# Kernel optimization log

Hardware: AMD Instinct MI355X
Metric: run time of the kernel (lower is better)

The kernel has to match this reference:

```python
import jax, jax.numpy as jnp
import numpy as np

N_HEADS = 8  # must match init_kwargs n_heads


def _shift(x, dy, dx):
    """out[..., y, x] = x[..., y+dy, x+dx], zero-padded outside. Replaces im2col gather / col2im scatter."""
    H, W = x.shape[-2], x.shape[-1]
    py0, py1 = max(dy, 0), max(-dy, 0)
    px0, px1 = max(dx, 0), max(-dx, 0)
    xp = jnp.pad(x, [(0, 0)] * (x.ndim - 2) + [(py1, py0), (px1, px0)])
    return xp[..., py1 + dy:py1 + dy + H, px1 + dx:px1 + dx + W]


def setup_inputs() -> dict:
    key = jax.random.key(0)
    k1, k2, k3 = jax.random.split(key, 3)
    N, D, H, W = 8, 256, 128, 128
    V = jax.random.normal(k1, (N, D, H, W), dtype=jnp.float32)
    K = jax.random.normal(k2, (N, D, H, W), dtype=jnp.float32)
    Q = jax.random.normal(k3, (N, D, H, W), dtype=jnp.float32)
    mask = jnp.ones((N, 1, H, W), dtype=jnp.float32)
    return {"V": V, "K": K, "Q": Q, "ksize": 5, "dilation": 1, "mask": mask}


def reference(V, K, Q, ksize, dilation, mask):
    N, D, H, W = Q.shape
    Dv = V.shape[1]
    nh = N_HEADS
    h_dim = D // nh
    dv_h = Dv // nh
    pad = (ksize // 2) * dilation
    offsets = [(i * dilation - pad, j * dilation - pad)
               for i in range(ksize) for j in range(ksize)]  # P = ksize**2 window positions

    # per-head QK scores for each window offset: score_p = sum_c K[y+dy, x+dx] * Q[y, x]
    Qh = Q.reshape(N, nh, h_dim, H, W)
    scores = []
    for (dy, dx) in offsets:
        Ks = _shift(K, dy, dx).reshape(N, nh, h_dim, H, W)
        scores.append(jnp.sum(Ks * Qh, axis=2))  # (N, nh, H, W)
    scores = jnp.stack(scores, axis=0)  # (P, N, nh, H, W)

    # softmax over window positions (dim 2 in the torch code), then mask
    att = jax.nn.softmax(scores, axis=0)
    m = mask.reshape(N, 1, H, W)[:, 0]  # (N, H, W)
    att = att * m[None, :, None, :, :]

    # diffuse V: value at (y, x) weighted by att[p] scatters to (y+dy, x+dx) (col2im add)
    Vh = V.reshape(N, nh, dv_h, H, W)
    out = jnp.zeros((N, nh, dv_h, H, W), dtype=V.dtype)
    for p, (dy, dx) in enumerate(offsets):
        contrib = Vh * att[p][:, :, None]  # (N, nh, dv_h, H, W)
        out = out + _shift(contrib, -dy, -dx)
    return out.reshape(N, Dv, H, W)
```

## Files before the change

### kernel.cpp

```cpp
#include <hip/hip_runtime.h>
#include <hip/hip_bf16.h>

typedef __hip_bfloat16 bf16;

#define N_     8
#define NH     8
#define HD     32
#define HW     (128 * 128)
#define H_     128
#define W_     128
#define P_     25
#define TY     8
#define RG     12
#define PITCH  136
#define CH     4
#define NCH    (HD / CH)
#define NPLANE (N_ * NH * HW)

static __device__ __forceinline__ unsigned short f2bf(float f) {
  bf16 b = __float2bfloat16(f);
  return *(unsigned short*)&b;
}

__global__ __launch_bounds__(256) void attn_kernel(
    const float* __restrict__ Kp, const float* __restrict__ Qp,
    const float* __restrict__ maskp, bf16* __restrict__ att) {
  __shared__ float L[CH][RG][PITCH];

  const int tid = threadIdx.x;
  const int y0 = blockIdx.x * TY, nh = blockIdx.y;
  const int ty = tid >> 5, g = tid & 31;
  const int gy = y0 + ty, gx0 = 4 * g;
  const float* KU = Kp + (size_t)nh * (HD * HW);
  const float* QU = Qp + (size_t)nh * (HD * HW);

  const int scol = tid & 127;
  const int sr0  = tid >> 7;
  int gofs[6]; bool okr[6];
#pragma unroll
  for (int j = 0; j < 6; ++j) {
    const int ky = y0 - 2 + sr0 + 2 * j;
    okr[j] = (unsigned)ky < H_;
    gofs[j] = okr[j] ? ky * W_ + scol : 0;
  }

  if (tid < 192) {
    const int ch = tid / 48, rem = tid % 48, r = rem >> 2, c = rem & 3;
    L[ch][r][c < 2 ? c : c + 128] = 0.f;
  }

  float s[P_][4];
#pragma unroll
  for (int p = 0; p < P_; ++p)
#pragma unroll
    for (int px = 0; px < 4; ++px) s[p][px] = 0.f;

  float t[6][CH];
#pragma unroll
  for (int j = 0; j < 6; ++j)
#pragma unroll
    for (int ch = 0; ch < CH; ++ch)
      t[j][ch] = okr[j] ? KU[gofs[j] + ch * HW] : 0.f;

#pragma unroll 1
  for (int kc = 0; kc < NCH; ++kc) {
    const int c0 = kc * CH;
    float q[CH][4];
#pragma unroll
    for (int ch = 0; ch < CH; ++ch) {
      float4 qv = *(const float4*)(QU + (c0 + ch) * HW + gy * W_ + gx0);
      q[ch][0] = qv.x; q[ch][1] = qv.y; q[ch][2] = qv.z; q[ch][3] = qv.w;
    }

    if (kc) __syncthreads();
#pragma unroll
    for (int j = 0; j < 6; ++j)
#pragma unroll
      for (int ch = 0; ch < CH; ++ch)
        L[ch][sr0 + 2 * j][scol + 2] = t[j][ch];
    __syncthreads();

    if (kc < NCH - 1) {
      const int cn = (kc + 1) * CH;
#pragma unroll
      for (int j = 0; j < 6; ++j)
#pragma unroll
        for (int ch = 0; ch < CH; ++ch)
          t[j][ch] = okr[j] ? KU[gofs[j] + (cn + ch) * HW] : 0.f;
    }

#pragma unroll
    for (int ch = 0; ch < CH; ++ch)
#pragma unroll
      for (int dyi = 0; dyi < 5; ++dyi) {
        const float* rp = &L[ch][ty + dyi][4 * g];
        float4 ra = *(const float4*)rp;
        float4 rb = *(const float4*)(rp + 4);
        float r[8] = {ra.x, ra.y, ra.z, ra.w, rb.x, rb.y, rb.z, rb.w};
#pragma unroll
        for (int dxi = 0; dxi < 5; ++dxi)
#pragma unroll
          for (int px = 0; px < 4; ++px)
            s[dyi * 5 + dxi][px] += r[px + dxi] * q[ch][px];
      }
  }

  float4 mv = *(const float4*)(maskp + (size_t)(nh >> 3) * HW + gy * W_ + gx0);
  float mvv[4] = {mv.x, mv.y, mv.z, mv.w};
  float inv[4];
#pragma unroll
  for (int px = 0; px < 4; ++px) {
    float m = s[0][px];
#pragma unroll
    for (int p = 1; p < P_; ++p) m = fmaxf(m, s[p][px]);
    float sum = 0.f;
#pragma unroll
    for (int p = 0; p < P_; ++p) { float e = __expf(s[p][px] - m); s[p][px] = e; sum += e; }
    inv[px] = mvv[px] / sum;
  }
  unsigned short* A = (unsigned short*)att;
  const size_t pixbase = (size_t)nh * HW + gy * W_ + gx0;
#pragma unroll
  for (int p = 0; p < P_; ++p) {
    uint2 o;
    o.x = (unsigned)f2bf(s[p][0] * inv[0]) | ((unsigned)f2bf(s[p][1] * inv[1]) << 16);
    o.y = (unsigned)f2bf(s[p][2] * inv[2]) | ((unsigned)f2bf(s[p][3] * inv[3]) << 16);
    *(uint2*)(A + (size_t)p * NPLANE + pixbase) = o;
  }
}

__global__ __launch_bounds__(256) void diffuse_kernel(
    const float* __restrict__ Vp, const bf16* __restrict__ att,
    float* __restrict__ out) {
  __shared__ float L[CH][RG][PITCH];

  const int tid = threadIdx.x;
  const int y0 = blockIdx.x * TY, nh = blockIdx.y;
  const int ty = tid >> 5, g = tid & 31;
  const int gy = y0 + ty, gx0 = 4 * g;
  const float* VU = Vp + (size_t)nh * (HD * HW);
  float* OU = out + (size_t)nh * (HD * HW);

  const int scol = tid & 127;
  const int sr0  = tid >> 7;
  int gofs[6]; bool okr[6];
#pragma unroll
  for (int j = 0; j < 6; ++j) {
    const int ky = y0 - 2 + sr0 + 2 * j;
    okr[j] = (unsigned)ky < H_;
    gofs[j] = okr[j] ? ky * W_ + scol : 0;
  }

  float t[6][CH];
#pragma unroll
  for (int j = 0; j < 6; ++j)
#pragma unroll
    for (int ch = 0; ch < CH; ++ch)
      t[j][ch] = okr[j] ? VU[gofs[j] + ch * HW] : 0.f;

  const unsigned short* A = (const unsigned short*)att;
  unsigned mxl[5], mxh[5];
#pragma unroll
  for (int exi = 0; exi < 5; ++exi) {
    bool o0 = (unsigned)(gx0 + 0 + exi - 2) < W_;
    bool o1 = (unsigned)(gx0 + 1 + exi - 2) < W_;
    bool o2 = (unsigned)(gx0 + 2 + exi - 2) < W_;
    bool o3 = (unsigned)(gx0 + 3 + exi - 2) < W_;
    mxl[exi] = (o0 ? 0xFFFFu : 0u) | (o1 ? 0xFFFF0000u : 0u);
    mxh[exi] = (o2 ? 0xFFFFu : 0u) | (o3 ? 0xFFFF0000u : 0u);
  }
  uint2 wp[P_];
#pragma unroll
  for (int j = 0; j < P_; ++j) {
    const int eyi = j / 5, exi = j % 5;
    const int ys = gy + eyi - 2;
    uint2 v; v.x = 0u; v.y = 0u;
    if ((unsigned)ys < H_) {
      const size_t base = (size_t)(24 - j) * NPLANE + (size_t)nh * HW +
                          (size_t)(ys * W_) + (gx0 + exi - 2);
      if (exi == 2) {
        v = *(const uint2*)(A + base);
      } else if ((exi & 1) == 0) {
        v.x = *(const unsigned*)(A + base);
        v.y = *(const unsigned*)(A + base + 2);
      } else {
        unsigned u0 = *(const unsigned*)(A + base - 1);
        unsigned u1 = *(const unsigned*)(A + base + 1);
        unsigned u2 = *(const unsigned*)(A + base + 3);
        v.x = (u0 >> 16) | (u1 << 16);
        v.y = (u1 >> 16) | (u2 << 16);
      }
    }
    v.x &= mxl[exi]; v.y &= mxh[exi];
    wp[j] = v;
  }

  if (tid < 192) {
    const int ch = tid / 48, rem = tid % 48, r = rem >> 2, c = rem & 3;
    L[ch][r][c < 2 ? c : c + 128] = 0.f;
  }

#pragma unroll 1
  for (int kc = 0; kc < NCH; ++kc) {
    if (kc) __syncthreads();
#pragma unroll
    for (int j = 0; j < 6; ++j)
#pragma unroll
      for (int ch = 0; ch < CH; ++ch)
        L[ch][sr0 + 2 * j][scol + 2] = t[j][ch];
    __syncthreads();

    if (kc < NCH - 1) {
      const int cn = (kc + 1) * CH;
#pragma unroll
      for (int j = 0; j < 6; ++j)
#pragma unroll
        for (int ch = 0; ch < CH; ++ch)
          t[j][ch] = okr[j] ? VU[gofs[j] + (cn + ch) * HW] : 0.f;
    }

    float acc[CH][4];
#pragma unroll
    for (int ch = 0; ch < CH; ++ch)
#pragma unroll
      for (int px = 0; px < 4; ++px) acc[ch][px] = 0.f;

#pragma unroll
    for (int eyi = 0; eyi < 5; ++eyi) {
      float vr[CH][8];
#pragma unroll
      for (int ch = 0; ch < CH; ++ch) {
        const float* rp = &L[ch][ty + eyi][4 * g];
        float4 ra = *(const float4*)rp;
        float4 rb = *(const float4*)(rp + 4);
        vr[ch][0] = ra.x; vr[ch][1] = ra.y; vr[ch][2] = ra.z; vr[ch][3] = ra.w;
        vr[ch][4] = rb.x; vr[ch][5] = rb.y; vr[ch][6] = rb.z; vr[ch][7] = rb.w;
      }
#pragma unroll
      for (int exi = 0; exi < 5; ++exi) {
        const uint2 w2 = wp[eyi * 5 + exi];
        float wf[4];
        wf[0] = __uint_as_float(w2.x << 16);
        wf[1] = __uint_as_float(w2.x & 0xFFFF0000u);
        wf[2] = __uint_as_float(w2.y << 16);
        wf[3] = __uint_as_float(w2.y & 0xFFFF0000u);
#pragma unroll
        for (int ch = 0; ch < CH; ++ch)
#pragma unroll
          for (int px = 0; px < 4; ++px)
            acc[ch][px] += wf[px] * vr[ch][px + exi];
      }
    }

    const int c0 = kc * CH;
#pragma unroll
    for (int ch = 0; ch < CH; ++ch) {
      float4 o = make_float4(acc[ch][0], acc[ch][1], acc[ch][2], acc[ch][3]);
      *(float4*)(OU + (c0 + ch) * HW + gy * W_ + gx0) = o;
    }
  }
}

extern "C" void kernel_launch(void* const* d_in, const int* in_sizes, int n_in,
                              void* d_out, int out_size, void* d_ws, size_t ws_size,
                              hipStream_t stream) {
  const float* V    = (const float*)d_in[0];
  const float* K    = (const float*)d_in[1];
  const float* Q    = (const float*)d_in[2];
  const float* mask = (const float*)d_in[5];

  bf16* att = (bf16*)d_ws;

  dim3 grid(H_ / TY, N_ * NH);
  attn_kernel<<<grid, 256, 0, stream>>>(K, Q, mask, att);
  diffuse_kernel<<<grid, 256, 0, stream>>>(V, att, (float*)d_out);
}
```

Baseline: 165.7 us.

## Use packed fp16 dot2 for QK scores and drop register prefetch of K

The score kernel now converts K and Q channel pairs to packed fp16 and accumulates scores with v_dot2 instructions, halving the shared-memory tile and the FMA count for the QK dot product. It also removes the register double-buffered prefetch of the next K chunk, loading K synchronously each iteration, and hoists the mask load to the start. This reduces ALU and LDS work but lowers score precision (fp16 with round-toward-zero) and may expose global load latency that the prefetch used to hide.

```diff
diff --git a/kernel.cpp b/kernel.cpp
--- a/kernel.cpp
+++ b/kernel.cpp
@@ -2,6 +2,8 @@
 #include <hip/hip_bf16.h>
 
 typedef __hip_bfloat16 bf16;
+typedef __attribute__((ext_vector_type(2))) __fp16    fp16x2;
+typedef __attribute__((ext_vector_type(2))) _Float16  half2t;
 
 #define N_     8
 #define NH     8
@@ -21,11 +23,20 @@
   bf16 b = __float2bfloat16(f);
   return *(unsigned short*)&b;
 }
+union h2u {
+  unsigned u; fp16x2 f; half2t h;
+};
+static __device__ __forceinline__ unsigned pk2u(float a, float b) {
+  h2u x; x.f = __builtin_amdgcn_cvt_pkrtz(a, b); return x.u;
+}
+static __device__ __forceinline__ half2t u2h(unsigned v) {
+  h2u x; x.u = v; return x.h;
+}
 
 __global__ __launch_bounds__(256) void attn_kernel(
     const float* __restrict__ Kp, const float* __restrict__ Qp,
     const float* __restrict__ maskp, bf16* __restrict__ att) {
-  __shared__ float L[CH][RG][PITCH];
+  __shared__ unsigned Lh[2][RG][PITCH];
 
   const int tid = threadIdx.x;
   const int y0 = blockIdx.x * TY, nh = blockIdx.y;
@@ -44,9 +55,9 @@
     gofs[j] = okr[j] ? ky * W_ + scol : 0;
   }
 
-  if (tid < 192) {
-    const int ch = tid / 48, rem = tid % 48, r = rem >> 2, c = rem & 3;
-    L[ch][r][c < 2 ? c : c + 128] = 0.f;
+  if (tid < 96) {
+    const int cp = tid / 48, rem = tid % 48, r = rem >> 2, c = rem & 3;
+    Lh[cp][r][c < 2 ? c : c + 128] = 0u;
   }
 
   float s[P_][4];
@@ -55,57 +66,56 @@
 #pragma unroll
     for (int px = 0; px < 4; ++px) s[p][px] = 0.f;
 
-  float t[6][CH];
-#pragma unroll
-  for (int j = 0; j < 6; ++j)
-#pragma unroll
-    for (int ch = 0; ch < CH; ++ch)
-      t[j][ch] = okr[j] ? KU[gofs[j] + ch * HW] : 0.f;
+  float4 mv = *(const float4*)(maskp + (size_t)(nh >> 3) * HW + gy * W_ + gx0);
 
 #pragma unroll 1
   for (int kc = 0; kc < NCH; ++kc) {
-    const int c0 = kc * CH;
+    const int cb = kc * CH;
+    if (kc) __syncthreads();
+
+    float t[6][CH];
+#pragma unroll
+    for (int j = 0; j < 6; ++j)
+#pragma unroll
+      for (int c = 0; c < CH; ++c)
+        t[j][c] = okr[j] ? KU[gofs[j] + (cb + c) * HW] : 0.f;
+#pragma unroll
+    for (int j = 0; j < 6; ++j)
+#pragma unroll
+      for (int m = 0; m < 2; ++m)
+        Lh[m][sr0 + 2 * j][scol + 2] = pk2u(t[j][2 * m], t[j][2 * m + 1]);
+    __syncthreads();
+
     float q[CH][4];
 #pragma unroll
-    for (int ch = 0; ch < CH; ++ch) {
-      float4 qv = *(const float4*)(QU + (c0 + ch) * HW + gy * W_ + gx0);
-      q[ch][0] = qv.x; q[ch][1] = qv.y; q[ch][2] = qv.z; q[ch][3] = qv.w;
-    }
-
-    if (kc) __syncthreads();
-#pragma unroll
-    for (int j = 0; j < 6; ++j)
-#pragma unroll
-      for (int ch = 0; ch < CH; ++ch)
-        L[ch][sr0 + 2 * j][scol + 2] = t[j][ch];
-    __syncthreads();
-
-    if (kc < NCH - 1) {
-      const int cn = (kc + 1) * CH;
-#pragma unroll
-      for (int j = 0; j < 6; ++j)
-#pragma unroll
-        for (int ch = 0; ch < CH; ++ch)
-          t[j][ch] = okr[j] ? KU[gofs[j] + (cn + ch) * HW] : 0.f;
-    }
-
-#pragma unroll
-    for (int ch = 0; ch < CH; ++ch)
+    for (int c = 0; c < CH; ++c) {
+      float4 qv = *(const float4*)(QU + (cb + c) * HW + gy * W_ + gx0);
+      q[c][0] = qv.x; q[c][1] = qv.y; q[c][2] = qv.z; q[c][3] = qv.w;
+    }
+    unsigned qp[2][4];
+#pragma unroll
+    for (int m = 0; m < 2; ++m)
+#pragma unroll
+      for (int px = 0; px < 4; ++px)
+        qp[m][px] = pk2u(q[2 * m][px], q[2 * m + 1][px]);
+
+#pragma unroll
+    for (int m = 0; m < 2; ++m)
 #pragma unroll
       for (int dyi = 0; dyi < 5; ++dyi) {
-        const float* rp = &L[ch][ty + dyi][4 * g];
-        float4 ra = *(const float4*)rp;
-        float4 rb = *(const float4*)(rp + 4);
-        float r[8] = {ra.x, ra.y, ra.z, ra.w, rb.x, rb.y, rb.z, rb.w};
+        const unsigned* rp = &Lh[m][ty + dyi][4 * g];
+        uint4 ra = *(const uint4*)rp;
+        uint4 rb = *(const uint4*)(rp + 4);
+        unsigned r[8] = {ra.x, ra.y, ra.z, ra.w, rb.x, rb.y, rb.z, rb.w};
 #pragma unroll
         for (int dxi = 0; dxi < 5; ++dxi)
 #pragma unroll
           for (int px = 0; px < 4; ++px)
-            s[dyi * 5 + dxi][px] += r[px + dxi] * q[ch][px];
-      }
-  }
-
-  float4 mv = *(const float4*)(maskp + (size_t)(nh >> 3) * HW + gy * W_ + gx0);
+            s[dyi * 5 + dxi][px] = __builtin_amdgcn_fdot2(
+                u2h(r[px + dxi]), u2h(qp[m][px]), s[dyi * 5 + dxi][px], false);
+      }
+  }
+
   float mvv[4] = {mv.x, mv.y, mv.z, mv.w};
   float inv[4];
 #pragma unroll
```

After: 169.2 us. 1.02x slower.
